# Optimization experiments

Hardware: AMD Instinct MI355X
Metric: run time of the kernel (lower is better)

Reference implementation:

```python
import jax, jax.numpy as jnp
import numpy as np

B, S, D, H = 8, 2048, 1024, 1024

def setup_inputs() -> dict:
    key = jax.random.key(0)
    ks = jax.random.split(key, 7)
    s = 1.0 / np.sqrt(D)  # torch Linear default init scale (uniform bound)
    x = jax.random.normal(ks[0], (B, S, D), dtype=jnp.float32)
    Wq = jax.random.uniform(ks[1], (D, H), jnp.float32, -s, s)
    bq = jax.random.uniform(ks[2], (H,), jnp.float32, -s, s)
    Wk = jax.random.uniform(ks[3], (D, H), jnp.float32, -s, s)
    bk = jax.random.uniform(ks[4], (H,), jnp.float32, -s, s)
    Wv = jax.random.uniform(ks[5], (D, H), jnp.float32, -s, s)
    bv = jax.random.uniform(ks[6], (H,), jnp.float32, -s, s)
    return {"x": x, "Wq": Wq, "bq": bq, "Wk": Wk, "bk": bk, "Wv": Wv, "bv": bv}

def reference(x, Wq, bq, Wk, bk, Wv, bv):
    scale = jnp.asarray(H ** 0.5, x.dtype)
    q = jnp.einsum('bsd,dh->bsh', x, Wq) + bq
    k = jnp.einsum('bsd,dh->bsh', x, Wk) + bk
    v = jnp.einsum('bsd,dh->bsh', x, Wv) + bv
    scores = jnp.einsum('bqh,bkh->bqk', q, k) / scale  # [B,S,S]
    probs = jax.nn.softmax(scores, axis=-1)
    return jnp.einsum('bqk,bkh->bqh', probs, v)
```

## Files before the change

### kernel.cpp

```cpp
#include <hip/hip_runtime.h>
#include <hip/hip_bf16.h>
#include <stdint.h>

using bf16 = __hip_bfloat16;
typedef __bf16 bf16x8 __attribute__((ext_vector_type(8)));
typedef unsigned int u32x4 __attribute__((ext_vector_type(4)));
typedef float f32x4 __attribute__((ext_vector_type(4)));

#define GLOAD_LDS16(gp, lp)                                                    \
  __builtin_amdgcn_global_load_lds(                                           \
      (const __attribute__((address_space(1))) void*)(gp),                     \
      (__attribute__((address_space(3))) void*)(lp), 16, 0, 0)

#define WAITCNT_VM(N) asm volatile("s_waitcnt vmcnt(" #N ")" ::: "memory")
#define SB0() __builtin_amdgcn_sched_barrier(0)

__device__ inline void store_out(bf16* p, float v)  { *p = __float2bfloat16(v); }
__device__ inline void store_out(float* p, float v) { *p = v; }

__device__ __forceinline__ bf16x8 ldsread16(const bf16* p) {
    u32x4 r = *reinterpret_cast<const u32x4*>(p);
    return __builtin_bit_cast(bf16x8, r);
}

template <typename OUT_T, int BIAS_AXIS, bool NFAST>
__global__ __launch_bounds__(256, 2) void gemm_bm(
    const bf16* __restrict__ A, const bf16* __restrict__ Bt,
    const float* __restrict__ bias0, const float* __restrict__ bias1,
    OUT_T* __restrict__ out0, OUT_T* __restrict__ out1, int Nsplit,
    int K, int lda, int ldb, int ldc,
    long long sA, long long sB, long long sC, float alpha)
{
    __shared__ __align__(16) bf16 lds[36864];

    const int Mt = gridDim.x, Nt = gridDim.y;
    const int nwg = Mt * Nt * gridDim.z;
    const int hw  = blockIdx.x + Mt * (blockIdx.y + Nt * blockIdx.z);
    const int lg  = (nwg & 7) ? hw : ((hw & 7) * (nwg >> 3) + (hw >> 3));
    const int per = Mt * Nt;
    const int zt  = lg / per;
    const int rem = lg - zt * per;
    int mt, nt;
    if (NFAST) { mt = rem / Nt; nt = rem - mt * Nt; }
    else       { mt = rem % Mt; nt = rem / Mt; }

    A  += (long long)zt * sA;
    Bt += (long long)zt * sB;
    out0 += (long long)zt * sC;
    if (out1) out1 += (long long)zt * sC;

    const int bm = mt * 256;
    const int bn = nt * 128;
    const int t = threadIdx.x, lane = t & 63, w = t >> 6;
    const int wm = w >> 1, wn = w & 1;
    const int fr = lane & 15, c16 = lane >> 4;

    const bf16* gA[4];
    const bf16* gB[2];
    #pragma unroll
    for (int k = 0; k < 4; ++k) {
        const int idx = t + 256 * k, r = idx >> 2, c = idx & 3;
        gA[k] = A + (long long)(bm + r) * lda + ((c ^ ((r >> 1) & 3)) << 3);
    }
    #pragma unroll
    for (int k = 0; k < 2; ++k) {
        const int idx = t + 256 * k, r = idx >> 2, c = idx & 3;
        gB[k] = Bt + (long long)(bn + r) * ldb + ((c ^ ((r >> 1) & 3)) << 3);
    }
    const int dstA = t * 8;
    const int dstB = 8192 + t * 8;

#define STAGE(JT, SLOTB) do {                                                  \
    GLOAD_LDS16(gA[0] + (JT) * 32, &lds[(SLOTB) + dstA]);                      \
    GLOAD_LDS16(gA[1] + (JT) * 32, &lds[(SLOTB) + dstA + 2048]);               \
    GLOAD_LDS16(gA[2] + (JT) * 32, &lds[(SLOTB) + dstA + 4096]);               \
    GLOAD_LDS16(gA[3] + (JT) * 32, &lds[(SLOTB) + dstA + 6144]);               \
    GLOAD_LDS16(gB[0] + (JT) * 32, &lds[(SLOTB) + dstB]);                      \
    GLOAD_LDS16(gB[1] + (JT) * 32, &lds[(SLOTB) + dstB + 2048]);               \
} while (0)

    const int swz8 = (c16 ^ ((fr >> 1) & 3)) << 3;
    const int offA = (wm * 128 + fr) * 32 + swz8;
    const int offB = 8192 + (wn * 64 + fr) * 32 + swz8;

    const int nk = K >> 5;

    STAGE(0, 0); STAGE(1, 12288);
    WAITCNT_VM(6);
    __builtin_amdgcn_s_barrier();

    f32x4 acc[8][4] = {};

    int slotb = 0;
    for (int j = 0; j < nk; ++j) {
        SB0();

        bf16x8 af[8], bfv[4];
        #pragma unroll
        for (int m = 0; m < 8; ++m)
            af[m] = ldsread16(&lds[slotb + offA + m * 512]);
        #pragma unroll
        for (int n = 0; n < 4; ++n)
            bfv[n] = ldsread16(&lds[slotb + offB + n * 512]);

        if (j + 2 < nk) {
            int s2 = slotb + 24576; if (s2 >= 36864) s2 -= 36864;
            STAGE(j + 2, s2);
        }

        #pragma unroll
        for (int m = 0; m < 8; ++m)
            #pragma unroll
            for (int n = 0; n < 4; ++n)
                acc[m][n] = __builtin_amdgcn_mfma_f32_16x16x32_bf16(
                    af[m], bfv[n], acc[m][n], 0, 0, 0);

        SB0();
        if (j + 2 < nk)      { WAITCNT_VM(6); }
        else if (j + 1 < nk) { WAITCNT_VM(0); }
        __builtin_amdgcn_s_barrier();

        slotb += 12288; if (slotb == 36864) slotb = 0;
    }

    const int colbase = bn + wn * 64 + fr;
    const int rowbase = bm + wm * 128 + c16 * 4;
    #pragma unroll
    for (int n = 0; n < 4; ++n) {
        const int gc = colbase + n * 16;
        const bool seg0 = gc < Nsplit;
        OUT_T* op = seg0 ? out0 : out1;
        const int col = seg0 ? gc : gc - Nsplit;
        float bcol = 0.0f;
        if (BIAS_AXIS == 0) {
            const float* bp = seg0 ? bias0 : bias1;
            if (bp) bcol = bp[col];
        }
        #pragma unroll
        for (int m = 0; m < 8; ++m) {
            #pragma unroll
            for (int jj = 0; jj < 4; ++jj) {
                const int row = rowbase + m * 16 + jj;
                float v = acc[m][n][jj] * alpha;
                if (BIAS_AXIS == 0) v += bcol;
                else if (bias0)     v += bias0[row];
                store_out(&op[(long long)row * ldc + col], v);
            }
        }
    }
#undef STAGE
}

__global__ __launch_bounds__(256) void f32_to_bf16(
    const float* __restrict__ in, bf16* __restrict__ out, long long n)
{
    long long i = ((long long)blockIdx.x * 256 + threadIdx.x) * 4;
    const long long stride = (long long)gridDim.x * 256 * 4;
    for (; i < n; i += stride) {
        float4 v = *reinterpret_cast<const float4*>(in + i);
        unsigned ux = __float_as_uint(v.x), uy = __float_as_uint(v.y);
        unsigned uz = __float_as_uint(v.z), uw = __float_as_uint(v.w);
        ushort4 o;
        o.x = (unsigned short)((ux + 0x7fffu + ((ux >> 16) & 1u)) >> 16);
        o.y = (unsigned short)((uy + 0x7fffu + ((uy >> 16) & 1u)) >> 16);
        o.z = (unsigned short)((uz + 0x7fffu + ((uz >> 16) & 1u)) >> 16);
        o.w = (unsigned short)((uw + 0x7fffu + ((uw >> 16) & 1u)) >> 16);
        *reinterpret_cast<ushort4*>(out + i) = o;
    }
}

__global__ void transpose_f32_bf16(const float* __restrict__ in,
                                   bf16* __restrict__ out, int R, int C)
{
    __shared__ float tile[32][33];
    const int c0 = blockIdx.x * 32, r0 = blockIdx.y * 32;
    const int tx = threadIdx.x, ty = threadIdx.y;
    #pragma unroll
    for (int i = ty; i < 32; i += 8)
        tile[i][tx] = in[(long long)(r0 + i) * C + (c0 + tx)];
    __syncthreads();
    #pragma unroll
    for (int i = ty; i < 32; i += 8)
        out[(long long)(c0 + i) * R + (r0 + tx)] = __float2bfloat16(tile[tx][i]);
}

__global__ __launch_bounds__(256) void softmax_rows(bf16* __restrict__ Sbuf, int cols)
{
    __shared__ float red[8];
    bf16* p = Sbuf + (long long)blockIdx.x * cols;
    const int t = threadIdx.x;

    u32x4 v = *reinterpret_cast<const u32x4*>(p + t * 8);
    float f[8];
    #pragma unroll
    for (int i = 0; i < 4; ++i) {
        f[2 * i]     = __uint_as_float(v[i] << 16);
        f[2 * i + 1] = __uint_as_float(v[i] & 0xffff0000u);
    }

    float m = -3.0e38f;
    #pragma unroll
    for (int i = 0; i < 8; ++i) m = fmaxf(m, f[i]);
    #pragma unroll
    for (int o = 32; o; o >>= 1) m = fmaxf(m, __shfl_xor(m, o));
    if ((t & 63) == 0) red[t >> 6] = m;
    __syncthreads();
    m = fmaxf(fmaxf(red[0], red[1]), fmaxf(red[2], red[3]));

    float s = 0.0f;
    #pragma unroll
    for (int i = 0; i < 8; ++i) { f[i] = __expf(f[i] - m); s += f[i]; }
    #pragma unroll
    for (int o = 32; o; o >>= 1) s += __shfl_xor(s, o);
    __syncthreads();
    if ((t & 63) == 0) red[4 + (t >> 6)] = s;
    __syncthreads();
    s = (red[4] + red[5]) + (red[6] + red[7]);
    const float inv = 1.0f / s;

    u32x4 o16;
    #pragma unroll
    for (int i = 0; i < 4; ++i) {
        unsigned ua = __float_as_uint(f[2 * i] * inv);
        unsigned ub = __float_as_uint(f[2 * i + 1] * inv);
        ua = (ua + 0x7fffu + ((ua >> 16) & 1u)) >> 16;
        ub = (ub + 0x7fffu + ((ub >> 16) & 1u)) & 0xffff0000u;
        o16[i] = ua | ub;
    }
    *reinterpret_cast<u32x4*>(p + t * 8) = o16;
}

extern "C" void kernel_launch(void* const* d_in, const int* in_sizes, int n_in,
                              void* d_out, int out_size, void* d_ws, size_t ws_size,
                              hipStream_t stream)
{
    const int B = 8, S = 2048, D = 1024, H = 1024;
    const float* x  = (const float*)d_in[0];
    const float* Wq = (const float*)d_in[1];
    const float* bq = (const float*)d_in[2];
    const float* Wk = (const float*)d_in[3];
    const float* bk = (const float*)d_in[4];
    const float* Wv = (const float*)d_in[5];
    const float* bv = (const float*)d_in[6];
    float* out = (float*)d_out;

    const size_t nQKV = (size_t)B * S * H;
    const size_t nW   = (size_t)D * H;
    const long long sSH = (long long)S * H;
    const long long sSS = (long long)S * S;

    dim3 tb(32, 8), g256(256);
    const float inv_scale = 1.0f / 32.0f;

    bf16* xb   = (bf16*)d_ws;
    bf16* Q    = xb  + nQKV;
    bf16* Kb   = Q   + nQKV;
    bf16* Vt   = Kb  + nQKV;
    bf16* WtQK = Vt  + nQKV;
    bf16* Wtv  = WtQK + 2 * nW;
    bf16* Sc   = Wtv + nW;

    const size_t tierA = (4 * nQKV + 3 * nW + (size_t)B * S * S) * 2;
    const size_t tierB = (4 * nQKV + 3 * nW + (size_t)S * S) * 2;
    const bool bigA = ws_size >= tierA;
    if (ws_size < tierB) return;

    f32_to_bf16<<<dim3(2048), g256, 0, stream>>>(x, xb, (long long)nQKV);
    transpose_f32_bf16<<<dim3(H / 32, D / 32), tb, 0, stream>>>(Wq, WtQK, D, H);
    transpose_f32_bf16<<<dim3(H / 32, D / 32), tb, 0, stream>>>(Wk, WtQK + nW, D, H);
    transpose_f32_bf16<<<dim3(H / 32, D / 32), tb, 0, stream>>>(Wv, Wtv, D, H);

    gemm_bm<bf16, 0, true><<<dim3(B * S / 256, 2 * H / 128, 1), g256, 0, stream>>>(
        xb, WtQK, bq, bk, Q, Kb, H, D, D, D, H, 0, 0, 0, 1.0f);

    gemm_bm<bf16, 1, false><<<dim3(H / 256, B * S / 128, 1), g256, 0, stream>>>(
        Wtv, xb, bv, nullptr, Vt, nullptr, 1 << 30, D, D, D, B * S, 0, 0, 0, 1.0f);

    if (bigA) {
        gemm_bm<bf16, 0, true><<<dim3(S / 256, S / 128, B), g256, 0, stream>>>(
            Q, Kb, nullptr, nullptr, Sc, nullptr, 1 << 30, H, H, H, S,
            sSH, sSH, sSS, inv_scale);
        softmax_rows<<<dim3(B * S), g256, 0, stream>>>(Sc, S);
        gemm_bm<float, 0, true><<<dim3(S / 256, H / 128, B), g256, 0, stream>>>(
            Sc, Vt, nullptr, nullptr, out, nullptr, 1 << 30, S, S, B * S, H,
            sSS, (long long)S, sSH, 1.0f);
    } else {
        for (int b = 0; b < B; ++b) {
            gemm_bm<bf16, 0, true><<<dim3(S / 256, S / 128, 1), g256, 0, stream>>>(
                Q + (size_t)b * sSH, Kb + (size_t)b * sSH, nullptr, nullptr,
                Sc, nullptr, 1 << 30, H, H, H, S, 0, 0, 0, inv_scale);
            softmax_rows<<<dim3(S), g256, 0, stream>>>(Sc, S);
            gemm_bm<float, 0, true><<<dim3(S / 256, H / 128, 1), g256, 0, stream>>>(
                Sc, Vt + (size_t)b * S, nullptr, nullptr,
                out + (size_t)b * sSH, nullptr, 1 << 30, S, S, B * S, H,
                0, 0, 0, 1.0f);
        }
    }
}
```

Measured before the change: 328.5 us.

## Switch GEMMs to 256x256 tiles with 8 waves and phased ping-pong pipeline

Replaces the 256x128, 4-wave GEMM with a 256x256, 512-thread, 8-wave kernel that consumes K in 64-wide double-buffered chunks. Each chunk is split into four phases that interleave LDS fragment reads, async global-to-LDS staging and MFMA bursts, with barriers and s_setprio raising wave priority during the MFMAs. The larger tile is meant to raise arithmetic intensity, cut global traffic per FLOP and overlap loads with compute. In exchange it uses 128KB of LDS per block and adds more barriers per K step, which may limit occupancy, and small grids like the V projection (4x64) produce fewer workgroups.

```diff
diff --git a/kernel.cpp b/kernel.cpp
--- a/kernel.cpp
+++ b/kernel.cpp
@@ -13,6 +13,7 @@
       (__attribute__((address_space(3))) void*)(lp), 16, 0, 0)
 
 #define WAITCNT_VM(N) asm volatile("s_waitcnt vmcnt(" #N ")" ::: "memory")
+#define WAITCNT_LGKM0() asm volatile("s_waitcnt lgkmcnt(0)" ::: "memory")
 #define SB0() __builtin_amdgcn_sched_barrier(0)
 
 __device__ inline void store_out(bf16* p, float v)  { *p = __float2bfloat16(v); }
@@ -24,14 +25,14 @@
 }
 
 template <typename OUT_T, int BIAS_AXIS, bool NFAST>
-__global__ __launch_bounds__(256, 2) void gemm_bm(
+__global__ __launch_bounds__(512, 2) void gemm8p(
     const bf16* __restrict__ A, const bf16* __restrict__ Bt,
     const float* __restrict__ bias0, const float* __restrict__ bias1,
     OUT_T* __restrict__ out0, OUT_T* __restrict__ out1, int Nsplit,
     int K, int lda, int ldb, int ldc,
     long long sA, long long sB, long long sC, float alpha)
 {
-    __shared__ __align__(16) bf16 lds[36864];
+    __shared__ __align__(16) bf16 lds[65536];
 
     const int Mt = gridDim.x, Nt = gridDim.y;
     const int nwg = Mt * Nt * gridDim.z;
@@ -49,78 +50,88 @@
     out0 += (long long)zt * sC;
     if (out1) out1 += (long long)zt * sC;
 
-    const int bm = mt * 256;
-    const int bn = nt * 128;
+    const int bm = mt * 256, bn = nt * 256;
     const int t = threadIdx.x, lane = t & 63, w = t >> 6;
-    const int wm = w >> 1, wn = w & 1;
+    const int wm = w >> 2, wn = w & 3;
     const int fr = lane & 15, c16 = lane >> 4;
 
-    const bf16* gA[4];
+    const bf16* gA[2];
     const bf16* gB[2];
     #pragma unroll
-    for (int k = 0; k < 4; ++k) {
-        const int idx = t + 256 * k, r = idx >> 2, c = idx & 3;
-        gA[k] = A + (long long)(bm + r) * lda + ((c ^ ((r >> 1) & 3)) << 3);
-    }
-    #pragma unroll
     for (int k = 0; k < 2; ++k) {
-        const int idx = t + 256 * k, r = idx >> 2, c = idx & 3;
-        gB[k] = Bt + (long long)(bn + r) * ldb + ((c ^ ((r >> 1) & 3)) << 3);
-    }
-    const int dstA = t * 8;
-    const int dstB = 8192 + t * 8;
-
-#define STAGE(JT, SLOTB) do {                                                  \
-    GLOAD_LDS16(gA[0] + (JT) * 32, &lds[(SLOTB) + dstA]);                      \
-    GLOAD_LDS16(gA[1] + (JT) * 32, &lds[(SLOTB) + dstA + 2048]);               \
-    GLOAD_LDS16(gA[2] + (JT) * 32, &lds[(SLOTB) + dstA + 4096]);               \
-    GLOAD_LDS16(gA[3] + (JT) * 32, &lds[(SLOTB) + dstA + 6144]);               \
-    GLOAD_LDS16(gB[0] + (JT) * 32, &lds[(SLOTB) + dstB]);                      \
-    GLOAD_LDS16(gB[1] + (JT) * 32, &lds[(SLOTB) + dstB + 2048]);               \
-} while (0)
-
-    const int swz8 = (c16 ^ ((fr >> 1) & 3)) << 3;
-    const int offA = (wm * 128 + fr) * 32 + swz8;
-    const int offB = 8192 + (wn * 64 + fr) * 32 + swz8;
-
-    const int nk = K >> 5;
-
-    STAGE(0, 0); STAGE(1, 12288);
-    WAITCNT_VM(6);
+        const int idx = t + 512 * k, r = idx >> 2, c = idx & 3;
+        const int cs = (c ^ ((r >> 1) & 3)) << 3;
+        gA[k] = A  + (long long)(bm + r) * lda + cs;
+        gB[k] = Bt + (long long)(bn + r) * ldb + cs;
+    }
+    const int d0 = t * 8, d1 = t * 8 + 4096;
+
+#define STG_A(T1, KH, SBASE) do {                                              \
+    GLOAD_LDS16(gA[0] + (T1) * 64 + (KH) * 32, &lds[(SBASE) + d0]);            \
+    GLOAD_LDS16(gA[1] + (T1) * 64 + (KH) * 32, &lds[(SBASE) + d1]);            \
+} while (0)
+#define STG_B(T1, KH, SBASE) do {                                              \
+    GLOAD_LDS16(gB[0] + (T1) * 64 + (KH) * 32, &lds[32768 + (SBASE) + d0]);    \
+    GLOAD_LDS16(gB[1] + (T1) * 64 + (KH) * 32, &lds[32768 + (SBASE) + d1]);    \
+} while (0)
+
+    const int swz  = (c16 ^ ((fr >> 1) & 3)) << 3;
+    const int offA0 = (wm * 128 + fr) * 32 + swz;
+    const int offB0 = (wn * 64 + fr) * 32 + swz;
+
+    f32x4 acc[8][4] = {};
+    bf16x8 af[4], bfv[4];
+
+#define RDA(H, SBASE) do {                                                     \
+    _Pragma("unroll") for (int mf = 0; mf < 4; ++mf)                           \
+        af[mf] = ldsread16(&lds[(SBASE) + offA0 + ((H) * 4 + mf) * 512]);      \
+} while (0)
+#define RDB(SBASE) do {                                                        \
+    _Pragma("unroll") for (int nf = 0; nf < 4; ++nf)                           \
+        bfv[nf] = ldsread16(&lds[32768 + (SBASE) + offB0 + nf * 512]);         \
+} while (0)
+#define MM(H) do {                                                             \
+    _Pragma("unroll") for (int mf = 0; mf < 4; ++mf)                           \
+        _Pragma("unroll") for (int nf = 0; nf < 4; ++nf)                       \
+            acc[(H) * 4 + mf][nf] = __builtin_amdgcn_mfma_f32_16x16x32_bf16(   \
+                af[mf], bfv[nf], acc[(H) * 4 + mf][nf], 0, 0, 0);              \
+} while (0)
+#define PH_MID(H) do {                                                         \
+    SB0(); __builtin_amdgcn_s_barrier();                                       \
+    WAITCNT_LGKM0(); SB0();                                                    \
+    __builtin_amdgcn_s_setprio(1); MM(H); __builtin_amdgcn_s_setprio(0);       \
+} while (0)
+#define PH_END() do { __builtin_amdgcn_s_barrier(); } while (0)
+
+    const int nk = K >> 6;
+
+    STG_A(0, 0, 0); STG_B(0, 0, 0);
+    STG_A(0, 1, 8192); STG_B(0, 1, 8192);
+    WAITCNT_VM(4);
     __builtin_amdgcn_s_barrier();
 
-    f32x4 acc[8][4] = {};
-
-    int slotb = 0;
-    for (int j = 0; j < nk; ++j) {
-        SB0();
-
-        bf16x8 af[8], bfv[4];
-        #pragma unroll
-        for (int m = 0; m < 8; ++m)
-            af[m] = ldsread16(&lds[slotb + offA + m * 512]);
-        #pragma unroll
-        for (int n = 0; n < 4; ++n)
-            bfv[n] = ldsread16(&lds[slotb + offB + n * 512]);
-
-        if (j + 2 < nk) {
-            int s2 = slotb + 24576; if (s2 >= 36864) s2 -= 36864;
-            STAGE(j + 2, s2);
+    for (int T = 0; T < nk; ++T) {
+        const int sb = (T & 1) << 14;
+        const int so = sb ^ 16384;
+        if (T + 1 < nk) {
+            RDA(0, sb); RDB(sb); STG_A(T + 1, 0, so);
+            PH_MID(0); WAITCNT_VM(4); PH_END();
+            RDA(1, sb); STG_B(T + 1, 0, so);
+            PH_MID(1); WAITCNT_VM(4); PH_END();
+            RDA(0, sb + 8192); RDB(sb + 8192); STG_A(T + 1, 1, so + 8192);
+            PH_MID(0); WAITCNT_VM(4); PH_END();
+            RDA(1, sb + 8192); STG_B(T + 1, 1, so + 8192);
+            PH_MID(1); WAITCNT_VM(4); PH_END();
+        } else {
+            RDA(0, sb); RDB(sb);
+            PH_MID(0); WAITCNT_VM(2); PH_END();
+            RDA(1, sb);
+            PH_MID(1); WAITCNT_VM(0); PH_END();
+            RDA(0, sb + 8192); RDB(sb + 8192);
+            PH_MID(0); PH_END();
+            RDA(1, sb + 8192);
+            PH_MID(1);
         }
-
-        #pragma unroll
-        for (int m = 0; m < 8; ++m)
-            #pragma unroll
-            for (int n = 0; n < 4; ++n)
-                acc[m][n] = __builtin_amdgcn_mfma_f32_16x16x32_bf16(
-                    af[m], bfv[n], acc[m][n], 0, 0, 0);
-
-        SB0();
-        if (j + 2 < nk)      { WAITCNT_VM(6); }
-        else if (j + 1 < nk) { WAITCNT_VM(0); }
-        __builtin_amdgcn_s_barrier();
-
-        slotb += 12288; if (slotb == 36864) slotb = 0;
     }
 
     const int colbase = bn + wn * 64 + fr;
@@ -148,7 +159,13 @@
             }
         }
     }
-#undef STAGE
+#undef STG_A
+#undef STG_B
+#undef RDA
+#undef RDB
+#undef MM
+#undef PH_MID
+#undef PH_END
 }
 
 __global__ __launch_bounds__(256) void f32_to_bf16(
@@ -249,7 +266,7 @@
     const long long sSH = (long long)S * H;
     const long long sSS = (long long)S * S;
 
-    dim3 tb(32, 8), g256(256);
+    dim3 tb(32, 8), g256(256), g512(512);
     const float inv_scale = 1.0f / 32.0f;
 
     bf16* xb   = (bf16*)d_ws;
@@ -270,27 +287,27 @@
     transpose_f32_bf16<<<dim3(H / 32, D / 32), tb, 0, stream>>>(Wk, WtQK + nW, D, H);
     transpose_f32_bf16<<<dim3(H / 32, D / 32), tb, 0, stream>>>(Wv, Wtv, D, H);
 
-    gemm_bm<bf16, 0, true><<<dim3(B * S / 256, 2 * H / 128, 1), g256, 0, stream>>>(
+    gemm8p<bf16, 0, true><<<dim3(B * S / 256, 2 * H / 256, 1), g512, 0, stream>>>(
         xb, WtQK, bq, bk, Q, Kb, H, D, D, D, H, 0, 0, 0, 1.0f);
 
-    gemm_bm<bf16, 1, false><<<dim3(H / 256, B * S / 128, 1), g256, 0, stream>>>(
+    gemm8p<bf16, 1, false><<<dim3(H / 256, B * S / 256, 1), g512, 0, stream>>>(
         Wtv, xb, bv, nullptr, Vt, nullptr, 1 << 30, D, D, D, B * S, 0, 0, 0, 1.0f);
 
     if (bigA) {
-        gemm_bm<bf16, 0, true><<<dim3(S / 256, S / 128, B), g256, 0, stream>>>(
+        gemm8p<bf16, 0, true><<<dim3(S / 256, S / 256, B), g512, 0, stream>>>(
             Q, Kb, nullptr, nullptr, Sc, nullptr, 1 << 30, H, H, H, S,
             sSH, sSH, sSS, inv_scale);
         softmax_rows<<<dim3(B * S), g256, 0, stream>>>(Sc, S);
-        gemm_bm<float, 0, true><<<dim3(S / 256, H / 128, B), g256, 0, stream>>>(
+        gemm8p<float, 0, true><<<dim3(S / 256, H / 256, B), g512, 0, stream>>>(
             Sc, Vt, nullptr, nullptr, out, nullptr, 1 << 30, S, S, B * S, H,
             sSS, (long long)S, sSH, 1.0f);
     } else {
         for (int b = 0; b < B; ++b) {
-            gemm_bm<bf16, 0, true><<<dim3(S / 256, S / 128, 1), g256, 0, stream>>>(
+            gemm8p<bf16, 0, true><<<dim3(S / 256, S / 256, 1), g512, 0, stream>>>(
                 Q + (size_t)b * sSH, Kb + (size_t)b * sSH, nullptr, nullptr,
                 Sc, nullptr, 1 << 30, H, H, H, S, 0, 0, 0, inv_scale);
             softmax_rows<<<dim3(S), g256, 0, stream>>>(Sc, S);
-            gemm_bm<float, 0, true><<<dim3(S / 256, H / 128, 1), g256, 0, stream>>>(
+            gemm8p<float, 0, true><<<dim3(S / 256, H / 256, 1), g512, 0, stream>>>(
                 Sc, Vt + (size_t)b * S, nullptr, nullptr,
                 out + (size_t)b * sSH, nullptr, 1 << 30, S, S, B * S, H,
                 0, 0, 0, 1.0f);
```

Result: slower. 1.277 ms (+288.7%).
